# Kernel tuning notes

Hardware: AMD Instinct MI355X
Metric: run time of the kernel (lower is better)

Reference implementation:

```python
import jax, jax.numpy as jnp
import numpy as np

N_NODES = 50000
NUM_LAYERS = 3
D = 128
NUM_LABELS = 16
NUM_EDGES = 1600000


def setup_inputs() -> dict:
    key = jax.random.key(0)
    ks = jax.random.split(key, 6)
    s = 1.0 / np.sqrt(D)
    x = jax.random.normal(ks[0], (N_NODES, D), dtype=jnp.float32)
    edge_index = jax.random.randint(ks[1], (2, NUM_EDGES), 0, N_NODES, dtype=jnp.int64)
    W1 = jax.random.normal(ks[2], (NUM_LAYERS, D, D), dtype=jnp.float32) * s
    b1 = jnp.zeros((NUM_LAYERS, D), dtype=jnp.float32)
    W2 = jax.random.normal(ks[3], (NUM_LAYERS, D, D), dtype=jnp.float32) * s
    b2 = jnp.zeros((NUM_LAYERS, D), dtype=jnp.float32)
    Wc = jax.random.normal(ks[4], (D, NUM_LABELS), dtype=jnp.float32) * s
    bc = jnp.zeros((NUM_LABELS,), dtype=jnp.float32)
    return {"x": x, "edge_index": edge_index, "W1": W1, "b1": b1,
            "W2": W2, "b2": b2, "Wc": Wc, "bc": bc}


def reference(x, edge_index, W1, b1, W2, b2, Wc, bc):
    # PyG GINConv (default eps=0): h_i = MLP((1+eps)*x_i + sum_{j->i} x_j)
    src, dst = edge_index[0], edge_index[1]
    h = x
    for l in range(NUM_LAYERS):
        agg = jax.ops.segment_sum(h[src], dst, num_segments=N_NODES)  # [N, D]
        z = h + agg
        h = jax.nn.relu(z @ W1[l] + b1[l]) @ W2[l] + b2[l]
    logits = h @ Wc + bc
    return (h, logits)
```

## Files before the change

### kernel.cpp

```cpp
#include <hip/hip_runtime.h>

#define DD 128
#define CHUNK 6144
#define NBMAX 512
#define SCAP 8192
#define PADSLACK 1024

typedef __attribute__((ext_vector_type(8))) short bf16x8;
typedef __attribute__((ext_vector_type(4))) float f32x4;

__device__ __forceinline__ unsigned bf16rne(float f) {
  unsigned u = __float_as_uint(f);
  return (u + 0x7FFFu + ((u >> 16) & 1u)) >> 16;
}
__device__ __forceinline__ unsigned packbf(float lo, float hi) {
  return bf16rne(lo) | (bf16rne(hi) << 16);
}
__device__ __forceinline__ float bflo(unsigned v) { return __uint_as_float(v << 16); }
__device__ __forceinline__ float bfhi(unsigned v) { return __uint_as_float(v & 0xFFFF0000u); }

__device__ void block_scan_incl(int* cnt, int* inc, int nb, int tid) {
  for (int i = tid; i < nb; i += 256) inc[i] = cnt[i];
  __syncthreads();
  for (int d = 1; d < nb; d <<= 1) {
    int i0 = tid, i1 = tid + 256;
    int v0 = 0, v1 = 0;
    if (i0 < nb && i0 >= d) v0 = inc[i0 - d];
    if (i1 < nb && i1 >= d) v1 = inc[i1 - d];
    __syncthreads();
    if (i0 < nb) inc[i0] += v0;
    if (i1 < nb) inc[i1] += v1;
    __syncthreads();
  }
}

__global__ __launch_bounds__(256) void s1_hist(const int* __restrict__ dst,
                                               int* __restrict__ bucketCount, int e) {
  __shared__ int h[NBMAX];
  int tid = threadIdx.x;
  for (int i = tid; i < NBMAX; i += 256) h[i] = 0;
  __syncthreads();
  int i0 = blockIdx.x * CHUNK;
  int i1 = min(i0 + CHUNK, e);
  for (int i = i0 + tid; i < i1; i += 256) atomicAdd(&h[dst[i] >> 7], 1);
  __syncthreads();
  for (int i = tid; i < NBMAX; i += 256)
    if (h[i]) atomicAdd(&bucketCount[i], h[i]);
}

__global__ __launch_bounds__(256) void s2_scan(const int* __restrict__ bucketCount,
                                               int* __restrict__ bucketOff,
                                               int* __restrict__ gCursor,
                                               int* __restrict__ rs, int nb, int n, int e) {
  __shared__ int cnt[NBMAX], inc[NBMAX];
  int tid = threadIdx.x;
  for (int i = tid; i < nb; i += 256) cnt[i] = bucketCount[i];
  __syncthreads();
  block_scan_incl(cnt, inc, nb, tid);
  for (int i = tid; i < nb; i += 256) {
    int off = inc[i] - cnt[i];
    bucketOff[i] = off;
    gCursor[i] = off;
  }
  if (tid == 0) { bucketOff[nb] = e; rs[n] = e; }
}

__global__ __launch_bounds__(256) void s3_scatter(const int* __restrict__ src,
                                                  const int* __restrict__ dst,
                                                  int* __restrict__ gCursor,
                                                  unsigned int* __restrict__ bucketed,
                                                  int e, int nb) {
  __shared__ int cnt[NBMAX], inc[NBMAX], base[NBMAX], cur[NBMAX];
  __shared__ unsigned int pairs[CHUNK];
  int tid = threadIdx.x;
  for (int i = tid; i < nb; i += 256) cnt[i] = 0;
  __syncthreads();
  int i0 = blockIdx.x * CHUNK;
  int i1 = min(i0 + CHUNK, e);
  for (int i = i0 + tid; i < i1; i += 256) atomicAdd(&cnt[dst[i] >> 7], 1);
  __syncthreads();
  block_scan_incl(cnt, inc, nb, tid);
  for (int b = tid; b < nb; b += 256) {
    int c = cnt[b];
    base[b] = c ? atomicAdd(&gCursor[b], c) : 0;
    cur[b] = inc[b] - c;
  }
  __syncthreads();
  for (int i = i0 + tid; i < i1; i += 256) {
    int d = dst[i];
    int p = atomicAdd(&cur[d >> 7], 1);
    pairs[p] = (unsigned)d | ((unsigned)src[i] << 16);
  }
  __syncthreads();
  int m = i1 - i0;
  for (int i = tid; i < m; i += 256) {
    unsigned w = pairs[i];
    int b = (int)(w & 0xFFFFu) >> 7;
    bucketed[base[b] + (i - (inc[b] - cnt[b]))] = w;
  }
}

__global__ __launch_bounds__(256) void s4_fill(const unsigned int* __restrict__ bucketed,
                                               const int* __restrict__ bucketOff,
                                               int* __restrict__ rs,
                                               unsigned short* __restrict__ pdeg,
                                               unsigned short* __restrict__ ssrc, int n) {
  __shared__ int cnt[128], pin[128], cur[128];
  __shared__ unsigned short outb[SCAP];
  int b = blockIdx.x;
  int bo = bucketOff[b], b1 = bucketOff[b + 1];
  int len = b1 - bo;
  int pstart = bo + b * PADSLACK;
  int tid = threadIdx.x;
  int n0 = b << 7;
  if (tid < 128) cnt[tid] = 0;
  __syncthreads();
  for (int i = tid; i < len; i += 256) atomicAdd(&cnt[bucketed[bo + i] & 127], 1);
  __syncthreads();
  int pc = 0;
  if (tid < 128) {
    pc = max(8, (cnt[tid] + 7) & ~7);
    pin[tid] = pc;
  }
  __syncthreads();
  for (int d = 1; d < 128; d <<= 1) {
    int v = 0;
    if (tid < 128 && tid >= d) v = pin[tid - d];
    __syncthreads();
    if (tid < 128) pin[tid] += v;
    __syncthreads();
  }
  int plen = pin[127];
  if (tid < 128) {
    int off = pin[tid] - pc;
    cur[tid] = off;
    int node = n0 + tid;
    if (node < n) {
      rs[node] = pstart + off;
      pdeg[node] = (unsigned short)pc;
    }
  }
  __syncthreads();
  if (plen <= SCAP) {
    for (int i = tid; i < plen; i += 256) outb[i] = (unsigned short)n;
    __syncthreads();
    for (int i = tid; i < len; i += 256) {
      unsigned w = bucketed[bo + i];
      int p = atomicAdd(&cur[w & 127], 1);
      outb[p] = (unsigned short)(w >> 16);
    }
    __syncthreads();
    for (int i = tid; i < plen; i += 256) ssrc[pstart + i] = outb[i];
  } else {
    for (int i = tid; i < plen; i += 256) ssrc[pstart + i] = (unsigned short)n;
    __syncthreads();
    for (int i = tid; i < len; i += 256) {
      unsigned w = bucketed[bo + i];
      int p = atomicAdd(&cur[w & 127], 1);
      ssrc[pstart + p] = (unsigned short)(w >> 16);
    }
  }
}

__global__ __launch_bounds__(256) void conv_bf16(const float* __restrict__ x,
                                                 unsigned int* __restrict__ hb,
                                                 int n64, int total64) {
  int i = blockIdx.x * 256 + threadIdx.x;
  if (i < n64) {
    float2 v = ((const float2*)x)[i];
    hb[i] = packbf(v.x, v.y);
  } else if (i < total64) {
    hb[i] = 0u;
  }
}

__global__ __launch_bounds__(256) void prep_w(const float* __restrict__ W1,
                                              const float* __restrict__ W2,
                                              short* __restrict__ wt) {
  int idx = blockIdx.x * 256 + threadIdx.x;
  if (idx >= 3 * 2 * 16384) return;
  int lm = idx >> 14;
  int e = idx & 16383;
  int k = e >> 7;
  int col = e & 127;
  int layer = lm >> 1, mat = lm & 1;
  const float* W = mat ? W2 : W1;
  float w = W[layer * 16384 + k * 128 + col];
  unsigned short h = (unsigned short)bf16rne(w);
  float hv = __uint_as_float((unsigned)h << 16);
  unsigned short lo = (unsigned short)bf16rne(w - hv);
  size_t base = (size_t)lm * 2 * 16384;
  int ksw = k ^ ((col & 7) << 3);
  wt[base + col * 128 + ksw] = (short)h;
  wt[base + 16384 + col * 128 + ksw] = (short)lo;
}

__global__ __launch_bounds__(256) void gather_zb(const unsigned int* __restrict__ hb,
                                                 const int* __restrict__ rs,
                                                 const unsigned short* __restrict__ pdeg,
                                                 const unsigned short* __restrict__ ssrc,
                                                 unsigned int* __restrict__ zb, int n) {
  int node = blockIdx.x * 4 + (threadIdx.x >> 6);
  if (node >= n) return;
  int lane = threadIdx.x & 63;
  int s0 = rs[node];
  int m = pdeg[node];
  unsigned v = hb[(unsigned)node * 64u + lane];
  float ax = bflo(v), ay = bfhi(v);
  unsigned A[8], B[8];
#pragma unroll
  for (int i = 0; i < 8; ++i)
    A[i] = hb[(unsigned)ssrc[s0 + i] * 64u + lane];
  int t1 = s0 + m;
  for (int t = s0 + 8; t < t1; t += 8) {
#pragma unroll
    for (int i = 0; i < 8; ++i)
      B[i] = hb[(unsigned)ssrc[t + i] * 64u + lane];
#pragma unroll
    for (int i = 0; i < 8; ++i) {
      ax += bflo(A[i]);
      ay += bfhi(A[i]);
    }
#pragma unroll
    for (int i = 0; i < 8; ++i) A[i] = B[i];
  }
#pragma unroll
  for (int i = 0; i < 8; ++i) {
    ax += bflo(A[i]);
    ay += bfhi(A[i]);
  }
  zb[(unsigned)node * 64u + lane] = packbf(ax, ay);
}

__global__ __launch_bounds__(256, 2) void mlp_mfma(
    const unsigned int* __restrict__ zb,
    const short* __restrict__ Wt1, const short* __restrict__ Wt2,
    const float* __restrict__ b1, const float* __restrict__ b2,
    float* __restrict__ fout, unsigned short* __restrict__ hbout, int n) {
  __shared__ char wbuf[32768];
  __shared__ char hsb[128 * 256];
  int tid = threadIdx.x;
  int w = tid >> 6, lane = tid & 63;
  int lr = lane & 15, hi = lane >> 4;
  int wr = (w & 1) * 64;
  int wc = (w >> 1) * 64;
  int node0 = blockIdx.x * 128;

  bf16x8 a[4][4];
#pragma unroll
  for (int t = 0; t < 4; ++t) {
    int row = node0 + wr + t * 16 + lr;
    row = min(row, n - 1);
    const char* rp = (const char*)(zb + (size_t)row * 64);
#pragma unroll
    for (int ks = 0; ks < 4; ++ks)
      a[t][ks] = *(const bf16x8*)(rp + ks * 64 + hi * 16);
  }

  f32x4 acc[4][4];
#pragma unroll
  for (int ct = 0; ct < 4; ++ct) {
    float bb = b1[wc + ct * 16 + lr];
#pragma unroll
    for (int t = 0; t < 4; ++t) acc[t][ct] = (f32x4){bb, bb, bb, bb};
  }

#pragma unroll
  for (int p = 0; p < 2; ++p) {
    __syncthreads();
    {
      const char* gs = (const char*)(Wt1 + p * 16384);
      for (int i = tid * 16; i < 32768; i += 256 * 16)
        *(float4*)&wbuf[i] = *(const float4*)(gs + i);
    }
    __syncthreads();
#pragma unroll
    for (int ct = 0; ct < 4; ++ct) {
      int col = wc + ct * 16 + lr;
      int cx = (col & 7) << 4;
#pragma unroll
      for (int ks = 0; ks < 4; ++ks) {
        bf16x8 b = *(const bf16x8*)&wbuf[(col * 256 + ks * 64 + hi * 16) ^ cx];
#pragma unroll
        for (int t = 0; t < 4; ++t)
          acc[t][ct] = __builtin_amdgcn_mfma_f32_16x16x32_bf16(a[t][ks], b, acc[t][ct], 0, 0, 0);
      }
    }
  }

#pragma unroll
  for (int t = 0; t < 4; ++t)
#pragma unroll
    for (int ct = 0; ct < 4; ++ct)
#pragma unroll
      for (int r = 0; r < 4; ++r) {
        int row = wr + t * 16 + hi * 4 + r;
        int col = wc + ct * 16 + lr;
        float v = fmaxf(acc[t][ct][r], 0.f);
        int byte = (row * 256 + col * 2) ^ ((row & 7) << 4);
        *(unsigned short*)&hsb[byte] = (unsigned short)bf16rne(v);
      }
  __syncthreads();

  bf16x8 a2[4][4];
#pragma unroll
  for (int t = 0; t < 4; ++t) {
    int row = wr + t * 16 + lr;
    int xr = (row & 7) << 4;
#pragma unroll
    for (int ks = 0; ks < 4; ++ks)
      a2[t][ks] = *(const bf16x8*)&hsb[(row * 256 + ks * 64 + hi * 16) ^ xr];
  }

#pragma unroll
  for (int ct = 0; ct < 4; ++ct) {
    float bb = b2[wc + ct * 16 + lr];
#pragma unroll
    for (int t = 0; t < 4; ++t) acc[t][ct] = (f32x4){bb, bb, bb, bb};
  }

#pragma unroll
  for (int p = 0; p < 2; ++p) {
    __syncthreads();
    {
      const char* gs = (const char*)(Wt2 + p * 16384);
      for (int i = tid * 16; i < 32768; i += 256 * 16)
        *(float4*)&wbuf[i] = *(const float4*)(gs + i);
    }
    __syncthreads();
#pragma unroll
    for (int ct = 0; ct < 4; ++ct) {
      int col = wc + ct * 16 + lr;
      int cx = (col & 7) << 4;
#pragma unroll
      for (int ks = 0; ks < 4; ++ks) {
        bf16x8 b = *(const bf16x8*)&wbuf[(col * 256 + ks * 64 + hi * 16) ^ cx];
#pragma unroll
        for (int t = 0; t < 4; ++t)
          acc[t][ct] = __builtin_amdgcn_mfma_f32_16x16x32_bf16(a2[t][ks], b, acc[t][ct], 0, 0, 0);
      }
    }
  }

#pragma unroll
  for (int t = 0; t < 4; ++t)
#pragma unroll
    for (int ct = 0; ct < 4; ++ct)
#pragma unroll
      for (int r = 0; r < 4; ++r) {
        int node = node0 + wr + t * 16 + hi * 4 + r;
        if (node < n) {
          int col = wc + ct * 16 + lr;
          float v = acc[t][ct][r];
          if (fout) fout[(size_t)node * DD + col] = v;
          if (hbout) hbout[(size_t)node * DD + col] = (unsigned short)bf16rne(v);
        }
      }
}

__global__ __launch_bounds__(256) void classifier_k(const float* __restrict__ h,
                                                    const float* __restrict__ Wc,
                                                    const float* __restrict__ bc,
                                                    float* __restrict__ out, int n) {
  __shared__ float wcs[DD * 16];
  for (int i = threadIdx.x; i < DD * 16; i += 256) wcs[i] = Wc[i];
  __syncthreads();
  int t = blockIdx.x * 256 + threadIdx.x;
  int node = t >> 4, c = t & 15;
  if (node >= n) return;
  float acc = bc[c];
  const float* hr = h + (size_t)node * DD;
#pragma unroll 8
  for (int k = 0; k < DD; ++k) acc += hr[k] * wcs[k * 16 + c];
  out[(size_t)node * 16 + c] = acc;
}

extern "C" void kernel_launch(void* const* d_in, const int* in_sizes, int n_in,
                              void* d_out, int out_size, void* d_ws, size_t ws_size,
                              hipStream_t stream) {
  const float* x = (const float*)d_in[0];
  const int* ei = (const int*)d_in[1];
  const float* W1 = (const float*)d_in[2];
  const float* b1 = (const float*)d_in[3];
  const float* W2 = (const float*)d_in[4];
  const float* b2 = (const float*)d_in[5];
  const float* Wc = (const float*)d_in[6];
  const float* bc = (const float*)d_in[7];

  const int N = in_sizes[0] / DD;
  const int E = in_sizes[1] / 2;
  const int* src = ei;
  const int* dst = ei + E;
  const int NB = (N + 127) >> 7;

  float* outp = (float*)d_out;
  float* h_final = outp;
  float* logits = outp + (size_t)N * DD;

  char* ws = (char*)d_ws;
  size_t off = 0;
  auto alloc = [&](size_t bytes) {
    char* p = ws + off;
    off = (off + bytes + 255) & ~(size_t)255;
    return p;
  };
  unsigned int* zb = (unsigned int*)alloc((size_t)N * 64 * 4);
  unsigned int* hb = (unsigned int*)alloc((size_t)(N + 1) * 64 * 4);
  short* wt = (short*)alloc((size_t)3 * 2 * 2 * 16384 * 2);
  int* bucketCount = (int*)alloc(NBMAX * 4);
  int* bucketOff = (int*)alloc((NBMAX + 1) * 4);
  int* gCursor = (int*)alloc(NBMAX * 4);
  int* rs = (int*)alloc((size_t)(N + 1) * 4);
  unsigned short* pdeg = (unsigned short*)alloc((size_t)N * 2);
  unsigned int* bucketed = (unsigned int*)alloc((size_t)E * 4);
  unsigned short* ssrc = (unsigned short*)alloc(((size_t)E + (size_t)NB * PADSLACK) * 2);

  const int gEdge = (E + CHUNK - 1) / CHUNK;
  const int gGather = (N + 3) / 4;
  const int gMlp = (N + 127) / 128;
  const int total64 = (N + 1) * 64;

  hipMemsetAsync(bucketCount, 0, NBMAX * 4, stream);
  s1_hist<<<gEdge, 256, 0, stream>>>(dst, bucketCount, E);
  s2_scan<<<1, 256, 0, stream>>>(bucketCount, bucketOff, gCursor, rs, NB, N, E);
  s3_scatter<<<gEdge, 256, 0, stream>>>(src, dst, gCursor, bucketed, E, NB);
  s4_fill<<<NB, 256, 0, stream>>>(bucketed, bucketOff, rs, pdeg, ssrc, N);

  prep_w<<<(3 * 2 * 16384 + 255) / 256, 256, 0, stream>>>(W1, W2, wt);
  conv_bf16<<<(total64 + 255) / 256, 256, 0, stream>>>(x, hb, N * 64, total64);

  auto WT = [&](int layer, int mat) { return wt + ((size_t)(layer * 2 + mat)) * 2 * 16384; };

  gather_zb<<<gGather, 256, 0, stream>>>(hb, rs, pdeg, ssrc, zb, N);
  mlp_mfma<<<gMlp, 256, 0, stream>>>(zb, WT(0, 0), WT(0, 1), b1, b2,
                                     nullptr, (unsigned short*)hb, N);
  gather_zb<<<gGather, 256, 0, stream>>>(hb, rs, pdeg, ssrc, zb, N);
  mlp_mfma<<<gMlp, 256, 0, stream>>>(zb, WT(1, 0), WT(1, 1), b1 + DD, b2 + DD,
                                     nullptr, (unsigned short*)hb, N);
  gather_zb<<<gGather, 256, 0, stream>>>(hb, rs, pdeg, ssrc, zb, N);
  mlp_mfma<<<gMlp, 256, 0, stream>>>(zb, WT(2, 0), WT(2, 1), b1 + 2 * DD, b2 + 2 * DD,
                                     h_final, nullptr, N);

  classifier_k<<<(N * 16 + 255) / 256, 256, 0, stream>>>(h_final, Wc, bc, logits, N);
}
```

Measured before the change: 295.2 us.

## Fuse classifier into final MLP kernel and widen gather unroll to 16

Drops the separate classifier kernel. The last mlp_mfma launch now stages its output tile in shared memory as bf16 and computes the 16 logits per node in place, which avoids re-reading h_final from global memory and saves one launch. The gather now pads each node's degree to a multiple of 16 and loads 16 neighbours at a time to get more memory loads in flight. In exchange, padding wastes more gather work on low-degree nodes (average about 32 here), the larger unroll raises register pressure, and the logits are computed from bf16-rounded h instead of fp32.

```diff
diff --git a/kernel.cpp b/kernel.cpp
--- a/kernel.cpp
+++ b/kernel.cpp
@@ -4,7 +4,7 @@
 #define CHUNK 6144
 #define NBMAX 512
 #define SCAP 8192
-#define PADSLACK 1024
+#define PADSLACK 2048
 
 typedef __attribute__((ext_vector_type(8))) short bf16x8;
 typedef __attribute__((ext_vector_type(4))) float f32x4;
@@ -119,7 +119,7 @@
   __syncthreads();
   int pc = 0;
   if (tid < 128) {
-    pc = max(8, (cnt[tid] + 7) & ~7);
+    pc = max(16, (cnt[tid] + 15) & ~15);
     pin[tid] = pc;
   }
   __syncthreads();
@@ -207,25 +207,25 @@
   int m = pdeg[node];
   unsigned v = hb[(unsigned)node * 64u + lane];
   float ax = bflo(v), ay = bfhi(v);
-  unsigned A[8], B[8];
-#pragma unroll
-  for (int i = 0; i < 8; ++i)
+  unsigned A[16], B[16];
+#pragma unroll
+  for (int i = 0; i < 16; ++i)
     A[i] = hb[(unsigned)ssrc[s0 + i] * 64u + lane];
   int t1 = s0 + m;
-  for (int t = s0 + 8; t < t1; t += 8) {
-#pragma unroll
-    for (int i = 0; i < 8; ++i)
+  for (int t = s0 + 16; t < t1; t += 16) {
+#pragma unroll
+    for (int i = 0; i < 16; ++i)
       B[i] = hb[(unsigned)ssrc[t + i] * 64u + lane];
 #pragma unroll
-    for (int i = 0; i < 8; ++i) {
+    for (int i = 0; i < 16; ++i) {
       ax += bflo(A[i]);
       ay += bfhi(A[i]);
     }
 #pragma unroll
-    for (int i = 0; i < 8; ++i) A[i] = B[i];
-  }
-#pragma unroll
-  for (int i = 0; i < 8; ++i) {
+    for (int i = 0; i < 16; ++i) A[i] = B[i];
+  }
+#pragma unroll
+  for (int i = 0; i < 16; ++i) {
     ax += bflo(A[i]);
     ay += bfhi(A[i]);
   }
@@ -236,7 +236,9 @@
     const unsigned int* __restrict__ zb,
     const short* __restrict__ Wt1, const short* __restrict__ Wt2,
     const float* __restrict__ b1, const float* __restrict__ b2,
-    float* __restrict__ fout, unsigned short* __restrict__ hbout, int n) {
+    float* __restrict__ fout, unsigned short* __restrict__ hbout,
+    const float* __restrict__ Wc, const float* __restrict__ bc,
+    float* __restrict__ lout, int n) {
   __shared__ char wbuf[32768];
   __shared__ char hsb[128 * 256];
   int tid = threadIdx.x;
@@ -356,23 +358,42 @@
           if (hbout) hbout[(size_t)node * DD + col] = (unsigned short)bf16rne(v);
         }
       }
-}
-
-__global__ __launch_bounds__(256) void classifier_k(const float* __restrict__ h,
-                                                    const float* __restrict__ Wc,
-                                                    const float* __restrict__ bc,
-                                                    float* __restrict__ out, int n) {
-  __shared__ float wcs[DD * 16];
-  for (int i = threadIdx.x; i < DD * 16; i += 256) wcs[i] = Wc[i];
-  __syncthreads();
-  int t = blockIdx.x * 256 + threadIdx.x;
-  int node = t >> 4, c = t & 15;
-  if (node >= n) return;
-  float acc = bc[c];
-  const float* hr = h + (size_t)node * DD;
-#pragma unroll 8
-  for (int k = 0; k < DD; ++k) acc += hr[k] * wcs[k * 16 + c];
-  out[(size_t)node * 16 + c] = acc;
+
+  if (lout) {
+    __syncthreads();
+    float* wcb = (float*)wbuf;
+    for (int i = tid; i < DD * 16; i += 256) wcb[i] = Wc[i];
+#pragma unroll
+    for (int t = 0; t < 4; ++t)
+#pragma unroll
+      for (int ct = 0; ct < 4; ++ct)
+#pragma unroll
+        for (int r = 0; r < 4; ++r) {
+          int row = wr + t * 16 + hi * 4 + r;
+          int col = wc + ct * 16 + lr;
+          int byte = (row * 256 + col * 2) ^ ((row & 7) << 4);
+          *(unsigned short*)&hsb[byte] = (unsigned short)bf16rne(acc[t][ct][r]);
+        }
+    __syncthreads();
+    int node = tid >> 1;
+    int lbase = (tid & 1) * 8;
+    float lacc[8];
+#pragma unroll
+    for (int j = 0; j < 8; ++j) lacc[j] = bc[lbase + j];
+    int xr = (node & 7) << 4;
+    for (int c = 0; c < DD; ++c) {
+      unsigned short hv16 = *(const unsigned short*)&hsb[(node * 256 + c * 2) ^ xr];
+      float hv = __uint_as_float((unsigned)hv16 << 16);
+      const float* wrow = &wcb[c * 16 + lbase];
+#pragma unroll
+      for (int j = 0; j < 8; ++j) lacc[j] += hv * wrow[j];
+    }
+    int gn = node0 + node;
+    if (gn < n) {
+#pragma unroll
+      for (int j = 0; j < 8; ++j) lout[(size_t)gn * 16 + lbase + j] = lacc[j];
+    }
+  }
 }
 
 extern "C" void kernel_launch(void* const* d_in, const int* in_sizes, int n_in,
@@ -433,13 +454,11 @@
 
   gather_zb<<<gGather, 256, 0, stream>>>(hb, rs, pdeg, ssrc, zb, N);
   mlp_mfma<<<gMlp, 256, 0, stream>>>(zb, WT(0, 0), WT(0, 1), b1, b2,
-                                     nullptr, (unsigned short*)hb, N);
+                                     nullptr, (unsigned short*)hb, nullptr, nullptr, nullptr, N);
   gather_zb<<<gGather, 256, 0, stream>>>(hb, rs, pdeg, ssrc, zb, N);
   mlp_mfma<<<gMlp, 256, 0, stream>>>(zb, WT(1, 0), WT(1, 1), b1 + DD, b2 + DD,
-                                     nullptr, (unsigned short*)hb, N);
+                                     nullptr, (unsigned short*)hb, nullptr, nullptr, nullptr, N);
   gather_zb<<<gGather, 256, 0, stream>>>(hb, rs, pdeg, ssrc, zb, N);
   mlp_mfma<<<gMlp, 256, 0, stream>>>(zb, WT(2, 0), WT(2, 1), b1 + 2 * DD, b2 + 2 * DD,
-                                     h_final, nullptr, N);
-
-  classifier_k<<<(N * 16 + 255) / 256, 256, 0, stream>>>(h_final, Wc, bc, logits, N);
-}
+                                     h_final, nullptr, Wc, bc, logits, N);
+}
```

Result: faster. 284.7 us (-3.6%).
